# Optimization experiments

Measured on AMD Instinct MI355X. Metric: run time of the kernel, lower is better.

The kernel has to match this reference:

```python
import jax, jax.numpy as jnp
import numpy as np

HIDDEN = 1024
HEADS = 16
BATCH = 2
SEQ = 2048
# dropout_p = 0.1 but module evaluated in eval mode (training=False) -> identity


def setup_inputs() -> dict:
    key = jax.random.key(0)
    k1, k2, k3 = jax.random.split(key, 3)
    x = jax.random.normal(k1, (BATCH, SEQ, HIDDEN), dtype=jnp.float32)
    # unit-scaling Linear: weight ~ N(0,1) (reset_parameters uses nn.init.normal_)
    w_qkv = jax.random.normal(k2, (3 * HIDDEN, HIDDEN), dtype=jnp.float32)
    w_o = jax.random.normal(k3, (HIDDEN, HIDDEN), dtype=jnp.float32)
    return {"x": x, "w_qkv": w_qkv, "w_o": w_o}


def reference(x, w_qkv, w_o):
    b, s, hid = x.shape
    heads = HEADS
    d = hid // heads
    # unit-scaled linear (constraint='to_output_scale'): y = x @ W.T * fan_in**-0.5
    qkv = (x @ w_qkv.T) * (hid ** -0.5)            # [b, s, 3*hid]
    # einops 'b s (z h d) -> z b h s d'
    qkv = qkv.reshape(b, s, 3, heads, d)
    q = jnp.transpose(qkv[:, :, 0], (0, 2, 1, 3))   # [b, h, s, d]
    k = jnp.transpose(qkv[:, :, 1], (0, 2, 1, 3))
    v = jnp.transpose(qkv[:, :, 2], (0, 2, 1, 3))
    # unit-scaled matmul: scale = inner_dim**-0.5
    scores = jnp.einsum('bhqd,bhkd->bhqk', q, k) * (d ** -0.5)  # [b, h, s, s]
    # unit-scaled softmax: output_scale = n / sqrt(n - 1)
    attn = jax.nn.softmax(scores, axis=-1) * (s / np.sqrt(s - 1.0))
    # dropout inactive (eval mode)
    out = jnp.einsum('bhqk,bhkd->bhqd', attn, v) * (s ** -0.5)  # inner dim = s
    out = jnp.transpose(out, (0, 2, 1, 3)).reshape(b, s, hid)   # 'b h s d -> b s (h d)'
    return (out @ w_o.T) * (hid ** -0.5)
```

## Files before the change

kernel.cpp:

```cpp
#include <hip/hip_runtime.h>

typedef unsigned short u16;
typedef _Float16 f16x8 __attribute__((ext_vector_type(8)));
typedef _Float16 f16x4 __attribute__((ext_vector_type(4)));
typedef float f32x4 __attribute__((ext_vector_type(4)));
typedef unsigned short u16x4 __attribute__((ext_vector_type(4)));

#define HID 1024
#define SEQ 2048
#define NH 16
#define DH 64

__device__ __forceinline__ u16 f2h(float f) {
  return __builtin_bit_cast(u16, (_Float16)f);
}
__device__ __forceinline__ f32x4 mfma_h(f16x8 a, f16x8 b, f32x4 c) {
  return __builtin_amdgcn_mfma_f32_16x16x32_f16(a, b, c, 0, 0, 0);
}
__device__ __forceinline__ f32x4 mfma_h16(f16x4 a, f16x4 b, f32x4 c) {
  return __builtin_amdgcn_mfma_f32_16x16x16f16(a, b, c, 0, 0, 0);
}
__device__ __forceinline__ float fexp2(float x) {
#if __has_builtin(__builtin_amdgcn_exp2f)
  return __builtin_amdgcn_exp2f(x);
#else
  return __expf(0.69314718f * x);
#endif
}
__device__ __forceinline__ void g2l16(const u16* g, u16* l) {
  __builtin_amdgcn_global_load_lds(
      (const __attribute__((address_space(1))) unsigned int*)g,
      (__attribute__((address_space(3))) unsigned int*)l, 16, 0, 0);
}

#define NX4 ((4096 * 1024) / 4)
#define NQ4 ((3072 * 1024) / 4)
#define NO4 ((1024 * 1024) / 4)
__global__ __launch_bounds__(256) void prep_kernel(
    const float* __restrict__ x, const float* __restrict__ wq,
    const float* __restrict__ wo,
    u16* __restrict__ x16, u16* __restrict__ wq16, u16* __restrict__ wo16) {
  int i = blockIdx.x * 256 + threadIdx.x;
  const float4 v = (i < NX4) ? ((const float4*)x)[i]
                 : (i < NX4 + NQ4) ? ((const float4*)wq)[i - NX4]
                 : ((const float4*)wo)[i - NX4 - NQ4];
  u16* dst = (i < NX4) ? &x16[(size_t)i * 4]
           : (i < NX4 + NQ4) ? &wq16[(size_t)(i - NX4) * 4]
           : &wo16[(size_t)(i - NX4 - NQ4) * 4];
  u16x4 o;
  o[0] = f2h(v.x); o[1] = f2h(v.y); o[2] = f2h(v.z); o[3] = f2h(v.w);
  *(u16x4*)dst = o;
}

__global__ __launch_bounds__(256, 3) void gemm_qkv(
    const u16* __restrict__ a16, const u16* __restrict__ b16,
    u16* __restrict__ qf, u16* __restrict__ kf, u16* __restrict__ vtf) {
  __shared__ __align__(16) u16 la[128 * 32], lb[128 * 32];
  const int t = threadIdx.x;
  const int lane = t & 63, w = t >> 6;
  const int wr = w >> 1, wc = w & 1;
  const int lr = lane & 15, lg = lane >> 4;
  const int br = blockIdx.x, bc = blockIdx.y;
  const f32x4 fzero = {0.f, 0.f, 0.f, 0.f};
  f32x4 acc[4][4];
#pragma unroll
  for (int i = 0; i < 4; ++i)
#pragma unroll
    for (int j = 0; j < 4; ++j) acc[i][j] = fzero;
  const int srow = t >> 2, scol = (t & 3) << 3;
  const u16* ga = a16 + (size_t)(br * 128 + srow) * HID + scol;
  const u16* gb = b16 + (size_t)(bc * 128 + srow) * HID + scol;
  const int lo16 = t * 8;
  for (int kk = 0; kk < HID; kk += 32) {
    g2l16(ga + kk, &la[lo16]);
    g2l16(ga + kk + (size_t)64 * HID, &la[lo16 + 2048]);
    g2l16(gb + kk, &lb[lo16]);
    g2l16(gb + kk + (size_t)64 * HID, &lb[lo16 + 2048]);
    __syncthreads();
    f16x8 ah[4], bh[4];
#pragma unroll
    for (int i = 0; i < 4; ++i)
      ah[i] = *(const f16x8*)&la[(wr * 64 + i * 16 + lr) * 32 + lg * 8];
#pragma unroll
    for (int j = 0; j < 4; ++j)
      bh[j] = *(const f16x8*)&lb[(wc * 64 + j * 16 + lr) * 32 + lg * 8];
#pragma unroll
    for (int i = 0; i < 4; ++i)
#pragma unroll
      for (int j = 0; j < 4; ++j) acc[i][j] = mfma_h(ah[i], bh[j], acc[i][j]);
    __syncthreads();
  }
  const int m0 = br * 128 + wr * 64, n0 = bc * 128 + wc * 64;
#pragma unroll
  for (int i = 0; i < 4; ++i)
#pragma unroll
    for (int j = 0; j < 4; ++j)
#pragma unroll
      for (int r = 0; r < 4; ++r) {
        int row = m0 + i * 16 + lg * 4 + r;
        int col = n0 + j * 16 + lr;
        float val = acc[i][j][r] * 0.03125f;
        int b = row >> 11, s = row & 2047;
        int z = col >> 10, hh = (col >> 6) & 15, d = col & 63;
        int bhid = b * NH + hh;
        if (z == 0) {
          qf[((size_t)bhid * SEQ + s) * DH + d] = f2h(val * 0.18033688f);
        } else if (z == 1) {
          kf[((size_t)bhid * SEQ + s) * DH + d] = f2h(val);
        } else {
          int kv = s & 63;
          int ct = kv >> 4, lgv = (kv >> 2) & 3, rv = kv & 3;
          int kvp = ((ct >> 1) << 5) | (lgv << 3) | ((ct & 1) << 2) | rv;
          int s2 = (s & ~63) | kvp;
          vtf[((size_t)bhid * DH + d) * SEQ + s2] = f2h(val);
        }
      }
}

__global__ __launch_bounds__(256, 2) void gemm_proj(
    const u16* __restrict__ a16, const u16* __restrict__ b16,
    float* __restrict__ out) {
  __shared__ __align__(16) u16 la[128 * 32];
  __shared__ __align__(16) u16 lb[64 * 32];
  const int t = threadIdx.x;
  const int lane = t & 63, w = t >> 6;
  const int wr = w >> 1, wc = w & 1;
  const int lr = lane & 15, lg = lane >> 4;
  const int br = blockIdx.x, bc = blockIdx.y;
  const f32x4 fzero = {0.f, 0.f, 0.f, 0.f};
  f32x4 acc[4][2];
#pragma unroll
  for (int i = 0; i < 4; ++i)
#pragma unroll
    for (int j = 0; j < 2; ++j) acc[i][j] = fzero;
  const int srow = t >> 2, scol = (t & 3) << 3;
  const u16* ga = a16 + (size_t)(br * 128 + srow) * HID + scol;
  const u16* gb = b16 + (size_t)(bc * 64 + srow) * HID + scol;
  const int lo16 = t * 8;
  for (int kk = 0; kk < HID; kk += 32) {
    g2l16(ga + kk, &la[lo16]);
    g2l16(ga + kk + (size_t)64 * HID, &la[lo16 + 2048]);
    g2l16(gb + kk, &lb[lo16]);
    __syncthreads();
    f16x8 ah[4], bh[2];
#pragma unroll
    for (int i = 0; i < 4; ++i)
      ah[i] = *(const f16x8*)&la[(wr * 64 + i * 16 + lr) * 32 + lg * 8];
#pragma unroll
    for (int j = 0; j < 2; ++j)
      bh[j] = *(const f16x8*)&lb[(wc * 32 + j * 16 + lr) * 32 + lg * 8];
#pragma unroll
    for (int i = 0; i < 4; ++i)
#pragma unroll
      for (int j = 0; j < 2; ++j)
        acc[i][j] = mfma_h(ah[i], bh[j], acc[i][j]);
    __syncthreads();
  }
  const int m0 = br * 128 + wr * 64, n0 = bc * 64 + wc * 32;
#pragma unroll
  for (int i = 0; i < 4; ++i)
#pragma unroll
    for (int j = 0; j < 2; ++j)
#pragma unroll
      for (int r = 0; r < 4; ++r) {
        int row = m0 + i * 16 + lg * 4 + r;
        int col = n0 + j * 16 + lr;
        out[(size_t)row * HID + col] = acc[i][j][r] * 0.03125f;
      }
}

__global__ __launch_bounds__(256, 2) void attn_kernel(
    const u16* __restrict__ qf, const u16* __restrict__ kf,
    const u16* __restrict__ vtf, u16* __restrict__ o16) {
  __shared__ __align__(16) u16 lk[2][64 * 64];
  __shared__ __align__(16) u16 lv[2][64 * 64];
  const int t = threadIdx.x;
  const int lane = t & 63, w = t >> 6;
  const int lr = lane & 15, lg = lane >> 4;
  const int bh = blockIdx.x, qt = blockIdx.y;
  const size_t base_qk = (size_t)bh * SEQ * DH;
  const size_t base_vt = (size_t)bh * DH * SEQ;

  f16x8 qfr[2][2];
#pragma unroll
  for (int rt = 0; rt < 2; ++rt)
#pragma unroll
    for (int ks = 0; ks < 2; ++ks)
      qfr[rt][ks] = *(const f16x8*)&qf[base_qk +
          (size_t)(qt * 128 + w * 32 + rt * 16 + lr) * DH + ks * 32 + lg * 8];

  f16x4 bI;
#pragma unroll
  for (int j = 0; j < 4; ++j) bI[j] = (_Float16)((lr == lg * 4 + j) ? 1.0f : 0.0f);

  const f32x4 fzero = {0.f, 0.f, 0.f, 0.f};
  f32x4 acc_o[2][4];
  float l_i[2][4];
#pragma unroll
  for (int rt = 0; rt < 2; ++rt)
#pragma unroll
    for (int r = 0; r < 4; ++r) l_i[rt][r] = 0.f;
#pragma unroll
  for (int rt = 0; rt < 2; ++rt)
#pragma unroll
    for (int ct = 0; ct < 4; ++ct) acc_o[rt][ct] = fzero;

  const int srow = t >> 3;
  const int scol = ((t & 7) ^ (srow & 7)) << 3;
  const int lo16 = t * 8;

  const u16* gk0 = kf + base_qk + (size_t)srow * DH + scol;
  const u16* gv0 = vtf + base_vt + (size_t)srow * SEQ + scol;

#define STAGE(buf, j)                                             \
  {                                                               \
    const u16* gk = gk0 + (size_t)(j) * 64 * DH;                  \
    g2l16(gk, &lk[buf][lo16]);                                    \
    g2l16(gk + 32 * DH, &lk[buf][lo16 + 2048]);                   \
    const u16* gv = gv0 + (j) * 64;                               \
    g2l16(gv, &lv[buf][lo16]);                                    \
    g2l16(gv + (size_t)32 * SEQ, &lv[buf][lo16 + 2048]);          \
  }

  STAGE(0, 0)

  for (int j = 0; j < SEQ / 64; ++j) {
    const int cur = j & 1;
    __syncthreads();

    f32x4 sa[2][4];
#pragma unroll
    for (int rt = 0; rt < 2; ++rt)
#pragma unroll
      for (int ct = 0; ct < 4; ++ct) sa[rt][ct] = fzero;
#pragma unroll
    for (int ks = 0; ks < 2; ++ks)
#pragma unroll
      for (int ct = 0; ct < 4; ++ct) {
        int row = ct * 16 + lr;
        f16x8 kfr = *(const f16x8*)&lk[cur][row * 64 + (((ks * 4 + lg) ^ (row & 7)) << 3)];
#pragma unroll
        for (int rt = 0; rt < 2; ++rt) sa[rt][ct] = mfma_h(qfr[rt][ks], kfr, sa[rt][ct]);
      }

    if (j + 1 < SEQ / 64) STAGE(cur ^ 1, j + 1)

    f16x8 pfr[2][2];
#pragma unroll
    for (int rt = 0; rt < 2; ++rt) {
      f32x4 tr[4];
#pragma unroll
      for (int ct = 0; ct < 4; ++ct) {
        f16x4 a4;
#pragma unroll
        for (int r = 0; r < 4; ++r) {
          float p = fexp2(sa[rt][ct][r]);
          l_i[rt][r] += p;
          a4[r] = (_Float16)p;
        }
        tr[ct] = mfma_h16(a4, bI, fzero);
      }
#pragma unroll
      for (int ks = 0; ks < 2; ++ks) {
        f16x8 pf;
#pragma unroll
        for (int j2 = 0; j2 < 8; ++j2)
          pf[j2] = (_Float16)tr[ks * 2 + (j2 >> 2)][j2 & 3];
        pfr[rt][ks] = pf;
      }
    }

#pragma unroll
    for (int ks = 0; ks < 2; ++ks)
#pragma unroll
      for (int ct = 0; ct < 4; ++ct) {
        int vrow = ct * 16 + lr;
        f16x8 vfr = *(const f16x8*)&lv[cur][vrow * 64 + (((ks * 4 + lg) ^ (vrow & 7)) << 3)];
#pragma unroll
        for (int rt = 0; rt < 2; ++rt) acc_o[rt][ct] = mfma_h(pfr[rt][ks], vfr, acc_o[rt][ct]);
      }
  }

#pragma unroll
  for (int rt = 0; rt < 2; ++rt)
#pragma unroll
    for (int r = 0; r < 4; ++r) {
      float l = l_i[rt][r];
      l += __shfl_xor(l, 1, 16);
      l += __shfl_xor(l, 2, 16);
      l += __shfl_xor(l, 4, 16);
      l += __shfl_xor(l, 8, 16);
      l_i[rt][r] = l;
    }

  const int b = bh >> 4, hh = bh & 15;
  const float fact = 1.00024426f;
#pragma unroll
  for (int rt = 0; rt < 2; ++rt)
#pragma unroll
    for (int r = 0; r < 4; ++r) {
      float inv = fact / l_i[rt][r];
      int s = qt * 128 + w * 32 + rt * 16 + lg * 4 + r;
#pragma unroll
      for (int ct = 0; ct < 4; ++ct) {
        int d = ct * 16 + lr;
        float val = acc_o[rt][ct][r] * inv;
        o16[((size_t)(b * SEQ + s)) * HID + hh * DH + d] = f2h(val);
      }
    }
}

extern "C" void kernel_launch(void* const* d_in, const int* in_sizes, int n_in,
                              void* d_out, int out_size, void* d_ws, size_t ws_size,
                              hipStream_t stream) {
  const float* x = (const float*)d_in[0];
  const float* w_qkv = (const float*)d_in[1];
  const float* w_o = (const float*)d_in[2];
  u16* ws = (u16*)d_ws;
  const size_t XS = (size_t)4096 * 1024;
  const size_t WQ = (size_t)3072 * 1024;
  const size_t WO = (size_t)1024 * 1024;
  u16* x16  = ws;           u16* wq16 = x16 + XS;
  u16* wo16 = wq16 + WQ;
  u16* q_f  = wo16 + WO;    u16* k_f  = q_f + XS;
  u16* vt_f = k_f + XS;     u16* o16  = vt_f + XS;

  prep_kernel<<<(NX4 + NQ4 + NO4) / 256, 256, 0, stream>>>(
      x, w_qkv, w_o, x16, wq16, wo16);
  gemm_qkv<<<dim3(32, 24), 256, 0, stream>>>(x16, wq16, q_f, k_f, vt_f);
  attn_kernel<<<dim3(32, 16), 256, 0, stream>>>(q_f, k_f, vt_f, o16);
  gemm_proj<<<dim3(32, 16), 256, 0, stream>>>(o16, wo16, (float*)d_out);
}
```

Measured before the change: 176.8 us.

## Split attention KV range across two blocks and add combine kernel

Splits the key/value sequence for each query tile into two halves handled by separate blocks via blockIdx.z. Each block writes its unnormalized fp16 partial output and row sums, and a new combine kernel adds the halves and normalizes. The goal is to double the attention grid from 512 blocks and raise the occupancy hint to 4, so more of the GPU is busy. In exchange it adds an extra kernel launch, extra global traffic for the partial outputs, and rounds unnormalized partials to fp16. That last part works only because no max-subtraction is used, so the partials can be summed directly.

After: 185.9 us. +5.1%, slower.

```diff
diff --git a/kernel.cpp b/kernel.cpp
--- a/kernel.cpp
+++ b/kernel.cpp
@@ -169,15 +169,17 @@
       }
 }
 
-__global__ __launch_bounds__(256, 2) void attn_kernel(
+__global__ __launch_bounds__(256, 4) void attn_kernel(
     const u16* __restrict__ qf, const u16* __restrict__ kf,
-    const u16* __restrict__ vtf, u16* __restrict__ o16) {
+    const u16* __restrict__ vtf, u16* __restrict__ opart,
+    float* __restrict__ lpart) {
   __shared__ __align__(16) u16 lk[2][64 * 64];
   __shared__ __align__(16) u16 lv[2][64 * 64];
   const int t = threadIdx.x;
   const int lane = t & 63, w = t >> 6;
   const int lr = lane & 15, lg = lane >> 4;
-  const int bh = blockIdx.x, qt = blockIdx.y;
+  const int bh = blockIdx.x, qt = blockIdx.y, kvh = blockIdx.z;
+  const int j0 = kvh * (SEQ / 128);
   const size_t base_qk = (size_t)bh * SEQ * DH;
   const size_t base_vt = (size_t)bh * DH * SEQ;
 
@@ -222,9 +224,9 @@
     g2l16(gv + (size_t)32 * SEQ, &lv[buf][lo16 + 2048]);          \
   }
 
-  STAGE(0, 0)
-
-  for (int j = 0; j < SEQ / 64; ++j) {
+  STAGE(0, j0)
+
+  for (int j = j0; j < j0 + SEQ / 128; ++j) {
     const int cur = j & 1;
     __syncthreads();
 
@@ -243,7 +245,7 @@
         for (int rt = 0; rt < 2; ++rt) sa[rt][ct] = mfma_h(qfr[rt][ks], kfr, sa[rt][ct]);
       }
 
-    if (j + 1 < SEQ / 64) STAGE(cur ^ 1, j + 1)
+    if (j + 1 < j0 + SEQ / 128) STAGE(cur ^ 1, j + 1)
 
     f16x8 pfr[2][2];
 #pragma unroll
@@ -294,20 +296,41 @@
     }
 
   const int b = bh >> 4, hh = bh & 15;
-  const float fact = 1.00024426f;
+  u16* op = opart + (size_t)kvh * (4096 * 1024);
+  float* lp = lpart + kvh * (32 * SEQ) + bh * SEQ;
 #pragma unroll
   for (int rt = 0; rt < 2; ++rt)
 #pragma unroll
     for (int r = 0; r < 4; ++r) {
-      float inv = fact / l_i[rt][r];
       int s = qt * 128 + w * 32 + rt * 16 + lg * 4 + r;
+      if (lr == 0) lp[s] = l_i[rt][r];
 #pragma unroll
       for (int ct = 0; ct < 4; ++ct) {
         int d = ct * 16 + lr;
-        float val = acc_o[rt][ct][r] * inv;
-        o16[((size_t)(b * SEQ + s)) * HID + hh * DH + d] = f2h(val);
+        op[((size_t)(b * SEQ + s)) * HID + hh * DH + d] = f2h(acc_o[rt][ct][r]);
       }
     }
+}
+
+__global__ __launch_bounds__(256) void combine_kernel(
+    u16* __restrict__ o0, const u16* __restrict__ o1,
+    const float* __restrict__ lpart) {
+  int i = blockIdx.x * 256 + threadIdx.x;
+  int e = i * 8;
+  int bs = e >> 10;
+  int hh = (e & 1023) >> 6;
+  int b = bs >> 11, s = bs & 2047;
+  int bh = b * NH + hh;
+  float l0 = lpart[bh * SEQ + s];
+  float l1 = lpart[32 * SEQ + bh * SEQ + s];
+  float inv = 1.00024426f / (l0 + l1);
+  f16x8 a = *(const f16x8*)&o0[e];
+  f16x8 c = *(const f16x8*)&o1[e];
+  f16x8 o;
+#pragma unroll
+  for (int j = 0; j < 8; ++j)
+    o[j] = (_Float16)(((float)a[j] + (float)c[j]) * inv);
+  *(f16x8*)&o0[e] = o;
 }
 
 extern "C" void kernel_launch(void* const* d_in, const int* in_sizes, int n_in,
@@ -323,11 +346,14 @@
   u16* x16  = ws;           u16* wq16 = x16 + XS;
   u16* wo16 = wq16 + WQ;
   u16* q_f  = wo16 + WO;    u16* k_f  = q_f + XS;
-  u16* vt_f = k_f + XS;     u16* o16  = vt_f + XS;
+  u16* vt_f = k_f + XS;
+  u16* o_p0 = vt_f + XS;    u16* o_p1 = o_p0 + XS;
+  float* l_p = (float*)(o_p1 + XS);
 
   prep_kernel<<<(NX4 + NQ4 + NO4) / 256, 256, 0, stream>>>(
       x, w_qkv, w_o, x16, wq16, wo16);
   gemm_qkv<<<dim3(32, 24), 256, 0, stream>>>(x16, wq16, q_f, k_f, vt_f);
-  attn_kernel<<<dim3(32, 16), 256, 0, stream>>>(q_f, k_f, vt_f, o16);
-  gemm_proj<<<dim3(32, 16), 256, 0, stream>>>(o16, wo16, (float*)d_out);
-}
+  attn_kernel<<<dim3(32, 16, 2), 256, 0, stream>>>(q_f, k_f, vt_f, o_p0, l_p);
+  combine_kernel<<<(int)(XS / 8 / 256), 256, 0, stream>>>(o_p0, o_p1, l_p);
+  gemm_proj<<<dim3(32, 16), 256, 0, stream>>>(o_p0, wo16, (float*)d_out);
+}
```
